# Kernel optimization log

Measured on AMD Instinct MI355X. Metric: run time of the kernel, lower is better.

Reference implementation:

```python
import jax, jax.numpy as jnp
import numpy as np

B, S, D, H = 2, 2048, 1024, 16
HD = D // H

def setup_inputs() -> dict:
    key = jax.random.key(0)
    ks = jax.random.split(key, 5)
    scale = 0.02
    return {
        "x": jax.random.normal(ks[0], (B, S, D), dtype=jnp.float32),
        "Wq": jax.random.normal(ks[1], (D, D), dtype=jnp.float32) * scale,
        "Wk": jax.random.normal(ks[2], (D, D), dtype=jnp.float32) * scale,
        "Wv": jax.random.normal(ks[3], (D, D), dtype=jnp.float32) * scale,
        "Wo": jax.random.normal(ks[4], (D, D), dtype=jnp.float32) * scale,
        "bo": jnp.zeros((D,), dtype=jnp.float32),
    }

def reference(x, Wq, Wk, Wv, Wo, bo):
    b, n, _ = x.shape
    h, hd = H, HD
    # QKV projections (torch Linear: x @ W.T)
    q = (x @ Wq.T).reshape(b, n, h, hd).transpose(0, 2, 1, 3)  # [b,h,n,hd]
    k = (x @ Wk.T).reshape(b, n, h, hd).transpose(0, 2, 1, 3)
    v = (x @ Wv.T).reshape(b, n, h, hd).transpose(0, 2, 1, 3)
    scores = jnp.einsum("bhqd,bhkd->bhqk", q, k) / jnp.sqrt(jnp.float32(hd))
    # causal mask: positions j > i masked out
    causal = jnp.tril(jnp.ones((n, n), dtype=bool))
    scores = jnp.where(causal, scores, jnp.float32(-jnp.inf))
    attn = jax.nn.softmax(scores, axis=-1)  # dropout p=0.0 (eval)
    ctx = jnp.einsum("bhqk,bhkd->bhqd", attn, v)
    ctx = ctx.transpose(0, 2, 1, 3).reshape(b, n, h * hd)
    return ctx @ Wo.T + bo
```

## Files before the change

kernel.cpp:

```cpp
#include <hip/hip_runtime.h>
#include <stdint.h>

typedef __attribute__((ext_vector_type(8))) short short8;
typedef __attribute__((ext_vector_type(4))) short s16x4;
typedef __attribute__((ext_vector_type(4))) float f32x4;

#define B_ 2
#define S_ 2048
#define D_ 1024
#define H_ 16
#define HD_ 64
#define BS_ (B_ * S_)
#define QKVN (3 * D_)
#define QKN 2048

#define NEGBIG (-1e30f)

__device__ __forceinline__ short f2bf(float f) {
    uint32_t u = __builtin_bit_cast(uint32_t, f);
    u = (u + 0x7FFFu + ((u >> 16) & 1u)) >> 16;
    return (short)u;
}

__device__ __forceinline__ void gload_lds16(const void* g, void* lds) {
    __builtin_amdgcn_global_load_lds(
        (const __attribute__((address_space(1))) void*)g,
        (__attribute__((address_space(3))) void*)lds, 16, 0, 0);
}

__global__ void castk(const float* __restrict__ s, short* __restrict__ d, int n8,
                      float scale) {
    int i = blockIdx.x * blockDim.x + threadIdx.x;
    int stride = gridDim.x * blockDim.x;
    for (; i < n8; i += stride) {
        const float* sp = s + (size_t)i * 8;
        short8 o;
#pragma unroll
        for (int j = 0; j < 8; ++j) o[j] = f2bf(sp[j] * scale);
        *(short8*)(d + (size_t)i * 8) = o;
    }
}

template <int MODE>
__global__ __launch_bounds__(256) void gemm_nt(
    const short* __restrict__ A, const short* __restrict__ Bt,
    void* __restrict__ Cout, const float* __restrict__ bias,
    short* __restrict__ vtg, int M, int N, int K) {
    __shared__ short As[128 * 64];
    __shared__ short Bs[128 * 64];
    const int tid = threadIdx.x;
    const int w = tid >> 6, l = tid & 63;
    const int lg = l >> 4, lr = l & 15;
    const int nbn = N >> 7;
    const int bm = blockIdx.x / nbn, bn = blockIdx.x % nbn;
    const int m0 = bm << 7, n0 = bn << 7;
    const int wm = (w >> 1) << 6, wn = (w & 1) << 6;

    f32x4 acc[4][4] = {};

    for (int kt = 0; kt < K; kt += 64) {
#pragma unroll
        for (int it = 0; it < 4; ++it) {
            int off = ((it * 4 + w) * 64 + l) * 16;
            int row = off >> 7;
            int scol = (off & 127) ^ ((row & 7) << 4);
            gload_lds16(A + (size_t)(m0 + row) * K + kt + (scol >> 1),
                        (char*)As + (it * 4 + w) * 1024);
            gload_lds16(Bt + (size_t)(n0 + row) * K + kt + (scol >> 1),
                        (char*)Bs + (it * 4 + w) * 1024);
        }
        __syncthreads();
        short8 af[4][2], bf[4][2];
#pragma unroll
        for (int f = 0; f < 4; ++f)
#pragma unroll
            for (int ks = 0; ks < 2; ++ks) {
                int ra = wm + f * 16 + lr;
                af[f][ks] = *(const short8*)((const char*)As + ra * 128 +
                                             ((lg * 16 + ks * 64) ^ ((ra & 7) << 4)));
                int rb = wn + f * 16 + lr;
                bf[f][ks] = *(const short8*)((const char*)Bs + rb * 128 +
                                             ((lg * 16 + ks * 64) ^ ((rb & 7) << 4)));
            }
#pragma unroll
        for (int mf = 0; mf < 4; ++mf)
#pragma unroll
            for (int nf = 0; nf < 4; ++nf)
#pragma unroll
                for (int ks = 0; ks < 2; ++ks)
                    acc[mf][nf] = __builtin_amdgcn_mfma_f32_16x16x32_bf16(
                        af[mf][ks], bf[nf][ks], acc[mf][nf], 0, 0, 0);
        __syncthreads();
    }

    if (MODE == 2 && n0 >= QKN) {
#pragma unroll
        for (int mf = 0; mf < 4; ++mf)
#pragma unroll
            for (int nf = 0; nf < 4; ++nf) {
                int col = n0 + wn + nf * 16 + lr - QKN;
                int hh = col >> 6, d = col & 63;
                int token = m0 + wm + mf * 16 + lg * 4;
                int b = token >> 11, tk = token & 2047;
                int t64 = tk & ~63, rem = tk & 63;
                int r32 = rem & 31;
                int pos = (rem >> 5) * 32 + ((r32 & 15) >> 2) * 8 + ((r32 >> 4) & 1) * 4;
                s16x4 o;
#pragma unroll
                for (int i = 0; i < 4; ++i) o[i] = f2bf(acc[mf][nf][i]);
                *(s16x4*)&vtg[((size_t)(b * 16 + hh) * 64 + d) * (size_t)S_ + t64 + pos] = o;
            }
        return;
    }

#pragma unroll
    for (int mf = 0; mf < 4; ++mf)
#pragma unroll
        for (int nf = 0; nf < 4; ++nf) {
            int col = n0 + wn + nf * 16 + lr;
            float bv = 0.f;
            if (MODE == 1) bv = bias[col];
#pragma unroll
            for (int i = 0; i < 4; ++i) {
                int row = m0 + wm + mf * 16 + lg * 4 + i;
                float v = acc[mf][nf][i] + bv;
                if (MODE == 1)
                    ((float*)Cout)[(size_t)row * N + col] = v;
                else
                    ((short*)Cout)[(size_t)row * QKN + col] = f2bf(v);
            }
        }
}

__global__ __launch_bounds__(256) void attn_fwd(const short* __restrict__ qkb,
                                                const short* __restrict__ vtg,
                                                short* __restrict__ ctx) {
    const int qt = (S_ / 64 - 1) - blockIdx.x;
    const int bh = blockIdx.y;
    const int b = bh >> 4, h = bh & 15;
    const int tid = threadIdx.x;
    const int w = tid >> 6, l = tid & 63;
    const int lg = l >> 4, lr = l & 15;
    const int q0w = qt * 64 + w * 16;

    __shared__ short Ks[2][64 * 64];
    __shared__ short Vt[2][64 * 64];

    const short* base = qkb + (size_t)(b * S_) * QKN + h * HD_;
    const short* kpg = base + D_;
    const short* vrow = vtg + (size_t)bh * 64 * S_;

    short8 qf[2];
    {
        const short* g = base + (size_t)(q0w + lr) * QKN + lg * 8;
        qf[0] = *(const short8*)g;
        qf[1] = *(const short8*)(g + 32);
    }

    float m2 = NEGBIG, lsum = 0.f;
    f32x4 cacc[4] = {};
    const int qabs = q0w + lr;

    auto stage = [&](int kb, int buf) {
#pragma unroll
        for (int it = 0; it < 2; ++it) {
            int off = ((it * 4 + w) * 64 + l) * 16;
            int row = off >> 7;
            int scol = (off & 127) ^ ((row & 7) << 4);
            gload_lds16(kpg + (size_t)(kb + row) * QKN + (scol >> 1),
                        (char*)Ks[buf] + (it * 4 + w) * 1024);
            gload_lds16(vrow + (size_t)row * S_ + kb + (scol >> 1),
                        (char*)Vt[buf] + (it * 4 + w) * 1024);
        }
    };

    stage(0, 0);
    __syncthreads();

    for (int kt = 0; kt <= qt; ++kt) {
        const int buf = kt & 1;
        if (kt < qt) stage((kt + 1) * 64, buf ^ 1);

        const char* ksb = (const char*)Ks[buf];
        const char* vtb = (const char*)Vt[buf];

        f32x4 sfr[4] = {};
#pragma unroll
        for (int f = 0; f < 4; ++f)
#pragma unroll
            for (int ks = 0; ks < 2; ++ks) {
                int r = f * 16 + lr;
                short8 kf = *(const short8*)(ksb + r * 128 +
                                             ((lg * 16 + ks * 64) ^ ((r & 7) << 4)));
                sfr[f] = __builtin_amdgcn_mfma_f32_16x16x32_bf16(kf, qf[ks], sfr[f], 0, 0, 0);
            }

        float sv[16];
        float tmax = NEGBIG;
        if (kt == qt) {
            const int kb = kt * 64;
#pragma unroll
            for (int f = 0; f < 4; ++f)
#pragma unroll
                for (int i = 0; i < 4; ++i) {
                    int kpo = kb + f * 16 + lg * 4 + i;
                    float s2 = (kpo <= qabs) ? sfr[f][i] : NEGBIG;
                    sv[f * 4 + i] = s2;
                    tmax = fmaxf(tmax, s2);
                }
        } else {
#pragma unroll
            for (int f = 0; f < 4; ++f)
#pragma unroll
                for (int i = 0; i < 4; ++i) {
                    float s2 = sfr[f][i];
                    sv[f * 4 + i] = s2;
                    tmax = fmaxf(tmax, s2);
                }
        }
        tmax = fmaxf(tmax, __shfl_xor(tmax, 16));
        tmax = fmaxf(tmax, __shfl_xor(tmax, 32));
        if (!__all(tmax - m2 <= 8.f)) {
            float mnew = fmaxf(m2, tmax);
            float crs = exp2f(m2 - mnew);
            m2 = mnew;
            lsum *= crs;
#pragma unroll
            for (int i = 0; i < 4; ++i) {
                float ci = __shfl(crs, lg * 4 + i);
#pragma unroll
                for (int nf = 0; nf < 4; ++nf) cacc[nf][i] *= ci;
            }
        }
        float psum = 0.f;
        short pb[16];
#pragma unroll
        for (int t = 0; t < 16; ++t) {
            float p = exp2f(sv[t] - m2);
            psum += p;
            pb[t] = f2bf(p);
        }
        lsum += psum;

        short8 pa[2];
#pragma unroll
        for (int ks = 0; ks < 2; ++ks)
#pragma unroll
            for (int j = 0; j < 8; ++j)
                pa[ks][j] = pb[(2 * ks + (j >> 2)) * 4 + (j & 3)];

#pragma unroll
        for (int nf = 0; nf < 4; ++nf) {
            int r = nf * 16 + lr;
#pragma unroll
            for (int ks = 0; ks < 2; ++ks) {
                short8 vf = *(const short8*)(vtb + r * 128 +
                                             ((ks * 64 + lg * 16) ^ ((r & 7) << 4)));
                cacc[nf] = __builtin_amdgcn_mfma_f32_16x16x32_bf16(pa[ks], vf, cacc[nf], 0, 0, 0);
            }
        }
        __syncthreads();
    }

    lsum += __shfl_xor(lsum, 16);
    lsum += __shfl_xor(lsum, 32);
    float inv = 1.0f / lsum;
#pragma unroll
    for (int i = 0; i < 4; ++i) {
        float li = __shfl(inv, lg * 4 + i);
        int srow = q0w + lg * 4 + i;
        short* o = ctx + (size_t)(b * S_ + srow) * D_ + h * HD_ + lr;
#pragma unroll
        for (int nf = 0; nf < 4; ++nf) o[nf * 16] = f2bf(cacc[nf][i] * li);
    }
}

extern "C" void kernel_launch(void* const* d_in, const int* in_sizes, int n_in,
                              void* d_out, int out_size, void* d_ws, size_t ws_size,
                              hipStream_t stream) {
    const float* x  = (const float*)d_in[0];
    const float* Wq = (const float*)d_in[1];
    const float* Wk = (const float*)d_in[2];
    const float* Wv = (const float*)d_in[3];
    const float* Wo = (const float*)d_in[4];
    const float* bo = (const float*)d_in[5];

    short* xb   = (short*)d_ws;
    short* Wqkv = xb + (size_t)BS_ * D_;
    short* Wob  = Wqkv + (size_t)QKVN * D_;
    short* qkb  = Wob + (size_t)D_ * D_;
    short* ctxb = qkb + (size_t)BS_ * QKN;
    short* vtg  = ctxb + (size_t)BS_ * D_;

    const float qscale = 0.125f * 1.44269504089f;
    castk<<<1024, 256, 0, stream>>>(x, xb, BS_ * D_ / 8, 1.0f);
    castk<<<512, 256, 0, stream>>>(Wq, Wqkv, D_ * D_ / 8, qscale);
    castk<<<512, 256, 0, stream>>>(Wk, Wqkv + D_ * D_, D_ * D_ / 8, 1.0f);
    castk<<<512, 256, 0, stream>>>(Wv, Wqkv + 2 * D_ * D_, D_ * D_ / 8, 1.0f);
    castk<<<512, 256, 0, stream>>>(Wo, Wob, D_ * D_ / 8, 1.0f);

    gemm_nt<2><<<dim3((BS_ / 128) * (QKVN / 128)), 256, 0, stream>>>(
        xb, Wqkv, qkb, nullptr, vtg, BS_, QKVN, D_);

    attn_fwd<<<dim3(S_ / 64, B_ * H_), 256, 0, stream>>>(qkb, vtg, ctxb);

    gemm_nt<1><<<dim3((BS_ / 128) * (D_ / 128)), 256, 0, stream>>>(
        ctxb, Wob, d_out, bo, nullptr, BS_, D_, D_);
}
```

Before: 233.8 us.

## Fuse cast kernels and streamline attention softmax and staging arithmetic

Merges the five separate fp32-to-bf16 cast launches into one kernel that writes the contiguous workspace, removing four launches. In the attention kernel, staging addresses are precomputed once and advanced by pointer increments. The cross-lane max shuffles now run only inside the rescale branch, and the lane-local max and sum use tree reductions. Probabilities are packed with the hardware v_cvt_pk_bf16_f32 instruction instead of manual rounding. The skip test now uses each lane's own max, which is still correct because any large jump in a row's true max shows up in at least one lane.

```diff
diff --git a/kernel.cpp b/kernel.cpp
--- a/kernel.cpp
+++ b/kernel.cpp
@@ -4,6 +4,7 @@
 typedef __attribute__((ext_vector_type(8))) short short8;
 typedef __attribute__((ext_vector_type(4))) short s16x4;
 typedef __attribute__((ext_vector_type(4))) float f32x4;
+typedef __attribute__((ext_vector_type(4))) uint32_t u32x4;
 
 #define B_ 2
 #define S_ 2048
@@ -13,6 +14,8 @@
 #define BS_ (B_ * S_)
 #define QKVN (3 * D_)
 #define QKN 2048
+#define XN8 (BS_ * D_ / 8)
+#define WN8 (D_ * D_ / 8)
 
 #define NEGBIG (-1e30f)
 
@@ -22,22 +25,43 @@
     return (short)u;
 }
 
+__device__ __forceinline__ uint32_t cvtpk_bf16(float lo, float hi) {
+    uint32_t r;
+    asm("v_cvt_pk_bf16_f32 %0, %1, %2" : "=v"(r) : "v"(lo), "v"(hi));
+    return r;
+}
+
 __device__ __forceinline__ void gload_lds16(const void* g, void* lds) {
     __builtin_amdgcn_global_load_lds(
         (const __attribute__((address_space(1))) void*)g,
         (__attribute__((address_space(3))) void*)lds, 16, 0, 0);
 }
 
-__global__ void castk(const float* __restrict__ s, short* __restrict__ d, int n8,
-                      float scale) {
+__global__ void castall(const float* __restrict__ x, const float* __restrict__ Wq,
+                        const float* __restrict__ Wk, const float* __restrict__ Wv,
+                        const float* __restrict__ Wo, short* __restrict__ dst,
+                        float qs) {
     int i = blockIdx.x * blockDim.x + threadIdx.x;
     int stride = gridDim.x * blockDim.x;
-    for (; i < n8; i += stride) {
-        const float* sp = s + (size_t)i * 8;
+    const int total = XN8 + 4 * WN8;
+    for (; i < total; i += stride) {
+        const float* s;
+        int loc;
+        float sc = 1.f;
+        if (i < XN8) {
+            s = x; loc = i;
+        } else {
+            int r = i - XN8;
+            int wi = r >> 17;
+            loc = r & (WN8 - 1);
+            s = (wi == 0) ? Wq : (wi == 1) ? Wk : (wi == 2) ? Wv : Wo;
+            if (wi == 0) sc = qs;
+        }
+        const float* sp = s + (size_t)loc * 8;
         short8 o;
 #pragma unroll
-        for (int j = 0; j < 8; ++j) o[j] = f2bf(sp[j] * scale);
-        *(short8*)(d + (size_t)i * 8) = o;
+        for (int j = 0; j < 8; ++j) o[j] = f2bf(sp[j] * sc);
+        *(short8*)(dst + (size_t)i * 8) = o;
     }
 }
 
@@ -157,29 +181,37 @@
         qf[1] = *(const short8*)(g + 32);
     }
 
+    int off0 = (w * 64 + l) * 16, off1 = ((4 + w) * 64 + l) * 16;
+    int row0 = off0 >> 7, row1 = off1 >> 7;
+    int sc0 = (off0 & 127) ^ ((row0 & 7) << 4);
+    int sc1 = (off1 & 127) ^ ((row1 & 7) << 4);
+    const short* kA = kpg + (size_t)row0 * QKN + (sc0 >> 1);
+    const short* kB = kpg + (size_t)row1 * QKN + (sc1 >> 1);
+    const short* vA = vrow + (size_t)row0 * S_ + (sc0 >> 1);
+    const short* vB = vrow + (size_t)row1 * S_ + (sc1 >> 1);
+    char* ldsKA[2] = {(char*)Ks[0] + w * 1024, (char*)Ks[1] + w * 1024};
+    char* ldsKB[2] = {(char*)Ks[0] + (4 + w) * 1024, (char*)Ks[1] + (4 + w) * 1024};
+    char* ldsVA[2] = {(char*)Vt[0] + w * 1024, (char*)Vt[1] + w * 1024};
+    char* ldsVB[2] = {(char*)Vt[0] + (4 + w) * 1024, (char*)Vt[1] + (4 + w) * 1024};
+
+    auto stage = [&](int buf) {
+        gload_lds16(kA, ldsKA[buf]);
+        gload_lds16(kB, ldsKB[buf]);
+        gload_lds16(vA, ldsVA[buf]);
+        gload_lds16(vB, ldsVB[buf]);
+        kA += 64 * QKN; kB += 64 * QKN; vA += 64; vB += 64;
+    };
+
     float m2 = NEGBIG, lsum = 0.f;
     f32x4 cacc[4] = {};
     const int qabs = q0w + lr;
 
-    auto stage = [&](int kb, int buf) {
-#pragma unroll
-        for (int it = 0; it < 2; ++it) {
-            int off = ((it * 4 + w) * 64 + l) * 16;
-            int row = off >> 7;
-            int scol = (off & 127) ^ ((row & 7) << 4);
-            gload_lds16(kpg + (size_t)(kb + row) * QKN + (scol >> 1),
-                        (char*)Ks[buf] + (it * 4 + w) * 1024);
-            gload_lds16(vrow + (size_t)row * S_ + kb + (scol >> 1),
-                        (char*)Vt[buf] + (it * 4 + w) * 1024);
-        }
-    };
-
-    stage(0, 0);
+    stage(0);
     __syncthreads();
 
     for (int kt = 0; kt <= qt; ++kt) {
         const int buf = kt & 1;
-        if (kt < qt) stage((kt + 1) * 64, buf ^ 1);
+        if (kt < qt) stage(buf ^ 1);
 
         const char* ksb = (const char*)Ks[buf];
         const char* vtb = (const char*)Vt[buf];
@@ -195,8 +227,7 @@
                 sfr[f] = __builtin_amdgcn_mfma_f32_16x16x32_bf16(kf, qf[ks], sfr[f], 0, 0, 0);
             }
 
-        float sv[16];
-        float tmax = NEGBIG;
+        float p[16];
         if (kt == qt) {
             const int kb = kt * 64;
 #pragma unroll
@@ -204,24 +235,24 @@
 #pragma unroll
                 for (int i = 0; i < 4; ++i) {
                     int kpo = kb + f * 16 + lg * 4 + i;
-                    float s2 = (kpo <= qabs) ? sfr[f][i] : NEGBIG;
-                    sv[f * 4 + i] = s2;
-                    tmax = fmaxf(tmax, s2);
+                    p[f * 4 + i] = (kpo <= qabs) ? sfr[f][i] : NEGBIG;
                 }
         } else {
 #pragma unroll
             for (int f = 0; f < 4; ++f)
 #pragma unroll
-                for (int i = 0; i < 4; ++i) {
-                    float s2 = sfr[f][i];
-                    sv[f * 4 + i] = s2;
-                    tmax = fmaxf(tmax, s2);
-                }
-        }
-        tmax = fmaxf(tmax, __shfl_xor(tmax, 16));
-        tmax = fmaxf(tmax, __shfl_xor(tmax, 32));
+                for (int i = 0; i < 4; ++i) p[f * 4 + i] = sfr[f][i];
+        }
+        float mx01 = fmaxf(fmaxf(p[0], p[1]), fmaxf(p[2], p[3]));
+        float mx23 = fmaxf(fmaxf(p[4], p[5]), fmaxf(p[6], p[7]));
+        float mx45 = fmaxf(fmaxf(p[8], p[9]), fmaxf(p[10], p[11]));
+        float mx67 = fmaxf(fmaxf(p[12], p[13]), fmaxf(p[14], p[15]));
+        float tmax = fmaxf(fmaxf(mx01, mx23), fmaxf(mx45, mx67));
+
         if (!__all(tmax - m2 <= 8.f)) {
-            float mnew = fmaxf(m2, tmax);
+            float rmax = fmaxf(tmax, __shfl_xor(tmax, 16));
+            rmax = fmaxf(rmax, __shfl_xor(rmax, 32));
+            float mnew = fmaxf(m2, rmax);
             float crs = exp2f(m2 - mnew);
             m2 = mnew;
             lsum *= crs;
@@ -232,22 +263,25 @@
                 for (int nf = 0; nf < 4; ++nf) cacc[nf][i] *= ci;
             }
         }
-        float psum = 0.f;
-        short pb[16];
-#pragma unroll
-        for (int t = 0; t < 16; ++t) {
-            float p = exp2f(sv[t] - m2);
-            psum += p;
-            pb[t] = f2bf(p);
-        }
-        lsum += psum;
+#pragma unroll
+        for (int t = 0; t < 16; ++t) p[t] = exp2f(p[t] - m2);
+        float s0 = (p[0] + p[1]) + (p[2] + p[3]);
+        float s1 = (p[4] + p[5]) + (p[6] + p[7]);
+        float s2 = (p[8] + p[9]) + (p[10] + p[11]);
+        float s3 = (p[12] + p[13]) + (p[14] + p[15]);
+        lsum += (s0 + s1) + (s2 + s3);
 
         short8 pa[2];
 #pragma unroll
-        for (int ks = 0; ks < 2; ++ks)
-#pragma unroll
-            for (int j = 0; j < 8; ++j)
-                pa[ks][j] = pb[(2 * ks + (j >> 2)) * 4 + (j & 3)];
+        for (int ks = 0; ks < 2; ++ks) {
+            u32x4 pw;
+#pragma unroll
+            for (int wd = 0; wd < 4; ++wd) {
+                int tb = (2 * ks + (wd >> 1)) * 4 + (wd & 1) * 2;
+                pw[wd] = cvtpk_bf16(p[tb], p[tb + 1]);
+            }
+            pa[ks] = __builtin_bit_cast(short8, pw);
+        }
 
 #pragma unroll
         for (int nf = 0; nf < 4; ++nf) {
@@ -293,11 +327,7 @@
     short* vtg  = ctxb + (size_t)BS_ * D_;
 
     const float qscale = 0.125f * 1.44269504089f;
-    castk<<<1024, 256, 0, stream>>>(x, xb, BS_ * D_ / 8, 1.0f);
-    castk<<<512, 256, 0, stream>>>(Wq, Wqkv, D_ * D_ / 8, qscale);
-    castk<<<512, 256, 0, stream>>>(Wk, Wqkv + D_ * D_, D_ * D_ / 8, 1.0f);
-    castk<<<512, 256, 0, stream>>>(Wv, Wqkv + 2 * D_ * D_, D_ * D_ / 8, 1.0f);
-    castk<<<512, 256, 0, stream>>>(Wo, Wob, D_ * D_ / 8, 1.0f);
+    castall<<<2048, 256, 0, stream>>>(x, Wq, Wk, Wv, Wo, (short*)d_ws, qscale);
 
     gemm_nt<2><<<dim3((BS_ / 128) * (QKVN / 128)), 256, 0, stream>>>(
         xb, Wqkv, qkb, nullptr, vtg, BS_, QKVN, D_);
```

Result: faster. 217.2 us (-7.1%).
